# Optimization experiments

Measured on AMD Instinct MI355X. Metric: run time of the kernel, lower is better.

The kernel has to match this reference:

```python
import jax, jax.numpy as jnp
import numpy as np

# CUBA-LIF constants (from LavaNetwork.__init__ with beta=0.95)
THRESHOLD = 1.0
CURRENT_DECAY = 1.0   # current[t] = (1-1.0)*current[t-1] + input[t] == input[t]
VOLTAGE_DECAY = 1.0 - 0.95  # = 0.05, so v[t] = 0.95*v[t-1] + cur[t]

N_INPUT, N_HIDDEN, N_OUTPUT = 512, 2048, 4 * 64
B, T = 32, 1024


def setup_inputs() -> dict:
    key = jax.random.key(0)
    kx, k1, k2, k3, k4 = jax.random.split(key, 5)
    x = (jax.random.uniform(kx, (B, N_INPUT, T)) < 0.1).astype(jnp.float32)
    # learned params (Linear with bias); small scale so spiking is reasonable
    w1 = jax.random.normal(k1, (N_HIDDEN, N_INPUT), dtype=jnp.float32) * (1.0 / np.sqrt(N_INPUT))
    b1 = jax.random.normal(k2, (N_HIDDEN,), dtype=jnp.float32) * 0.01
    w2 = jax.random.normal(k3, (N_OUTPUT, N_HIDDEN), dtype=jnp.float32) * (1.0 / np.sqrt(N_HIDDEN))
    b2 = jax.random.normal(k4, (N_OUTPUT,), dtype=jnp.float32) * 0.01
    return {"x": x, "w1": w1, "b1": b1, "w2": w2, "b2": b2}


def _cuba_lif(cur):
    """CUBA neuron with current_decay=1 (current==synaptic input),
    leaky-integrate voltage, fire at threshold, reset voltage to 0.
    cur: (B, N, T) -> spikes (B, N, T)."""
    beta_v = 1.0 - VOLTAGE_DECAY  # 0.95

    def step(v, c_t):
        v = v * beta_v + c_t
        s = (v >= THRESHOLD).astype(v.dtype)
        v = v * (1.0 - s)  # reset-to-zero on spike (Loihi behavior)
        return v, s

    cur_t = jnp.moveaxis(cur, -1, 0)  # (T, B, N)
    v0 = jnp.zeros(cur.shape[:-1], cur.dtype)
    _, spk = jax.lax.scan(step, v0, cur_t)
    return jnp.moveaxis(spk, 0, -1)  # (B, N, T)


def reference(x, w1, b1, w2, b2):
    # layer 1: synapse (einsum 'bit,oi->bot' + bias) -> CUBA neuron
    cur1 = jnp.einsum('bit,oi->bot', x, w1) + b1[None, :, None]
    spk1 = _cuba_lif(cur1)
    # layer 2
    cur2 = jnp.einsum('bit,oi->bot', spk1, w2) + b2[None, :, None]
    spk2 = _cuba_lif(cur2)
    return (spk1, spk2)
```

## Files before the change

### kernel.cpp

```cpp
#include <hip/hip_runtime.h>


typedef int i32x4 __attribute__((ext_vector_type(4)));
typedef _Float16 f16x8 __attribute__((ext_vector_type(8)));
typedef _Float16 f16x4 __attribute__((ext_vector_type(4)));
typedef float f32x4 __attribute__((ext_vector_type(4)));

#define GLDS(g, l) __builtin_amdgcn_global_load_lds( \
    (const __attribute__((address_space(1))) void*)(g), \
    (__attribute__((address_space(3))) void*)(l), 16, 0, 0)

#define INV231 4.656612873077392578125e-10


__global__ __launch_bounds__(256) void prep_w8(const float* __restrict__ A,
                                               signed char* __restrict__ wp,
                                               int M, int K)
{
    long gt = (long)blockIdx.x * 256 + threadIdx.x;
    int kq4 = K >> 2;
    int m = (int)(gt / kq4), kq = (int)(gt % kq4);
    int k0 = kq * 4;
    int kt = k0 >> 6, kin = k0 & 63;
    int cw = ((kin >> 4) ^ (m >> 1)) & 3;
    float4 w = *(const float4*)&A[(long)m * K + k0];
    float wv[4] = {w.x, w.y, w.z, w.w};
    int pack[4] = {0, 0, 0, 0};
#pragma unroll
    for (int e = 0; e < 4; e++) {
        long k64 = (long)rint((double)wv[e] * 2147483648.0);
#pragma unroll
        for (int j = 0; j < 3; j++) {
            long r = ((k64 + 128) & 255) - 128;
            pack[j] |= ((int)r & 255) << (e * 8);
            k64 = (k64 - r) >> 8;
        }
        pack[3] |= ((int)k64 & 255) << (e * 8);
    }
#pragma unroll
    for (int p = 0; p < 4; p++)
        *(int*)&wp[(((long)kt * 4 + p) * M + m) * 64 + cw * 16 + (kin & 15)] = pack[p];
}

__global__ __launch_bounds__(256) void prep_x8(const float* __restrict__ x,
                                               unsigned char* __restrict__ xt)
{
    __shared__ float xs[64][68];
    const int b = blockIdx.z, i0 = blockIdx.y * 64, t0 = blockIdx.x * 64;
    const float* xb = x + ((long)b * 512 + i0) * 1024 + t0;
#pragma unroll
    for (int p = 0; p < 4; p++) {
        int f = threadIdx.x + p * 256;
        int i = f >> 4, t4 = (f & 15) * 4;
        *(float4*)&xs[i][t4] = *(const float4*)&xb[(long)i * 1024 + t4];
    }
    __syncthreads();
    int tt = threadIdx.x >> 2, c = threadIdx.x & 3;
    unsigned char bytes[16];
#pragma unroll
    for (int j = 0; j < 16; j++)
        bytes[j] = (unsigned char)xs[c * 16 + j][tt];
    *(uint4*)&xt[(((long)b * 8 + (i0 >> 6)) * 1024 + t0 + tt) * 64 + c * 16] =
        *(uint4*)bytes;
}

template <bool TRANS>
__global__ __launch_bounds__(256, 3) void gemm_i8(
    const signed char* __restrict__ wp,
    const unsigned char* __restrict__ act,
    const float* __restrict__ bias,
    float* __restrict__ C,
    int M, int K)
{
    __shared__ signed char Ws[2][4][32][64];

    const int b = blockIdx.z;
    const int m0 = blockIdx.x * 32, t0 = blockIdx.y * 128;
    const int tid = threadIdx.x, lane = tid & 63, wave = tid >> 6;
    const int wt = t0 + wave * 32;
    const int lm = lane & 15, lq = lane >> 4;
    const int fro = ((lq ^ (lm >> 1)) & 3) * 16;
    const int gl_t = lane >> 2, gl_c = (lane & 3) * 16;
    const int niter = K >> 6;

    const unsigned char* ab = act + (long)b * niter * 1024 * 64;
    const int p0 = wave >> 1, s0 = wave & 1;
    const int p1 = (wave + 4) >> 1, s1 = wave & 1;

    i32x4 acc[4][2][2];
#pragma unroll
    for (int p = 0; p < 4; p++)
#pragma unroll
        for (int i = 0; i < 2; i++)
#pragma unroll
            for (int j = 0; j < 2; j++) acc[p][i][j] = (i32x4)0;

    {
        const signed char* g0 = wp + (((long)p0) * M + m0 + s0 * 16 + gl_t) * 64 + gl_c;
        const signed char* g1 = wp + (((long)p1) * M + m0 + s1 * 16 + gl_t) * 64 + gl_c;
        GLDS(g0, &Ws[0][p0][s0 * 16][0]);
        GLDS(g1, &Ws[0][p1][s1 * 16][0]);
    }
    i32x4 a0 = *(const i32x4*)&ab[((long)(wt + 0 * 16 + lm)) * 64 + lq * 16];
    i32x4 a1 = *(const i32x4*)&ab[((long)(wt + 1 * 16 + lm)) * 64 + lq * 16];
    __syncthreads();

    for (int it = 0; it < niter; it++) {
        const int buf = it & 1;
        const int nx = (it + 1 < niter) ? it + 1 : it;
        if (it + 1 < niter) {
            const long kb = (long)(it + 1) * 4;
            const signed char* g0 =
                wp + ((kb + p0) * M + m0 + s0 * 16 + gl_t) * 64 + gl_c;
            const signed char* g1 =
                wp + ((kb + p1) * M + m0 + s1 * 16 + gl_t) * 64 + gl_c;
            GLDS(g0, &Ws[buf ^ 1][p0][s0 * 16][0]);
            GLDS(g1, &Ws[buf ^ 1][p1][s1 * 16][0]);
        }
        i32x4 an0 = *(const i32x4*)&ab[((long)nx * 1024 + wt + 0 * 16 + lm) * 64 + lq * 16];
        i32x4 an1 = *(const i32x4*)&ab[((long)nx * 1024 + wt + 1 * 16 + lm) * 64 + lq * 16];

#pragma unroll
        for (int p = 0; p < 4; p++) {
            i32x4 w0 = *(const i32x4*)&Ws[buf][p][lm][fro];
            i32x4 w1 = *(const i32x4*)&Ws[buf][p][16 + lm][fro];
            if (TRANS) {
                acc[p][0][0] = __builtin_amdgcn_mfma_i32_16x16x64_i8(a0, w0, acc[p][0][0], 0, 0, 0);
                acc[p][0][1] = __builtin_amdgcn_mfma_i32_16x16x64_i8(a0, w1, acc[p][0][1], 0, 0, 0);
                acc[p][1][0] = __builtin_amdgcn_mfma_i32_16x16x64_i8(a1, w0, acc[p][1][0], 0, 0, 0);
                acc[p][1][1] = __builtin_amdgcn_mfma_i32_16x16x64_i8(a1, w1, acc[p][1][1], 0, 0, 0);
            } else {
                acc[p][0][0] = __builtin_amdgcn_mfma_i32_16x16x64_i8(w0, a0, acc[p][0][0], 0, 0, 0);
                acc[p][0][1] = __builtin_amdgcn_mfma_i32_16x16x64_i8(w0, a1, acc[p][0][1], 0, 0, 0);
                acc[p][1][0] = __builtin_amdgcn_mfma_i32_16x16x64_i8(w1, a0, acc[p][1][0], 0, 0, 0);
                acc[p][1][1] = __builtin_amdgcn_mfma_i32_16x16x64_i8(w1, a1, acc[p][1][1], 0, 0, 0);
            }
        }
        __syncthreads();
        a0 = an0; a1 = an1;
    }

    if (TRANS) {
        double bv[2];
        bv[0] = (double)bias[m0 + lm];
        bv[1] = (double)bias[m0 + 16 + lm];
        float* Cb = C + (long)b * 1024 * M;
#pragma unroll
        for (int tf = 0; tf < 2; tf++)
#pragma unroll
            for (int r = 0; r < 4; r++) {
                const int trow = wt + tf * 16 + lq * 4 + r;
#pragma unroll
                for (int mf = 0; mf < 2; mf++) {
                    long T = acc[3][tf][mf][r];
                    T = T * 256 + acc[2][tf][mf][r];
                    T = T * 256 + acc[1][tf][mf][r];
                    T = T * 256 + acc[0][tf][mf][r];
                    Cb[(long)trow * M + m0 + mf * 16 + lm] =
                        (float)((double)T * INV231 + bv[mf]);
                }
            }
    } else {
        float* Cb = C + (long)b * M * 1024;
#pragma unroll
        for (int mf = 0; mf < 2; mf++)
#pragma unroll
            for (int r = 0; r < 4; r++) {
                const int mrow = m0 + mf * 16 + lq * 4 + r;
                const double bv = (double)bias[mrow];
#pragma unroll
                for (int tf = 0; tf < 2; tf++) {
                    long T = acc[3][mf][tf][r];
                    T = T * 256 + acc[2][mf][tf][r];
                    T = T * 256 + acc[1][mf][tf][r];
                    T = T * 256 + acc[0][mf][tf][r];
                    Cb[(long)mrow * 1024 + wt + tf * 16 + lm] =
                        (float)((double)T * INV231 + bv);
                }
            }
    }
}


__global__ __launch_bounds__(256) void lif1_t(
    const float* __restrict__ ct,
    unsigned char* __restrict__ spk8,
    unsigned* __restrict__ mask_ws)
{
    const int b = blockIdx.y;
    const int m = blockIdx.x * 256 + threadIdx.x;
    const float* src = ct + (long)b * 1024 * 2048 + m;
    unsigned char* spb = spk8 + (((long)b * 32 + (m >> 6)) * 1024) * 64 + (m & 63);
    unsigned* mw = mask_ws + (long)b * 32 * 2048 + m;
    double v = 0.0;
    for (int tw = 0; tw < 32; tw++) {
        float c[32];
#pragma unroll
        for (int j = 0; j < 32; j++)
            c[j] = src[(long)(tw * 32 + j) * 2048];
        unsigned mword = 0;
#pragma unroll
        for (int j = 0; j < 32; j++) {
            v = 0.95 * v + (double)c[j];
            bool s = v >= 1.0;
            mword |= (s ? 1u : 0u) << j;
            if (s) v = 0.0;
            spb[(long)(tw * 32 + j) * 64] = s ? 1 : 0;
        }
        mw[(long)tw * 2048] = mword;
    }
}

__global__ __launch_bounds__(256) void expand_spk(
    const unsigned* __restrict__ mask_ws,
    float* __restrict__ spk1)
{
    __shared__ unsigned msk[8][32];
    const long rowbase = (long)blockIdx.x * 8;
    const int b = (int)(rowbase >> 11), m0 = (int)(rowbase & 2047);
    const int tid = threadIdx.x;
    {
        int w = tid >> 3, r = tid & 7;
        msk[r][w] = mask_ws[((long)b * 32 + w) * 2048 + m0 + r];
    }
    __syncthreads();
    const int r = tid >> 5, l5 = tid & 31;
    float* dst = spk1 + (rowbase + r) * 1024;
    const int sh = (l5 & 7) * 4;
#pragma unroll
    for (int j = 0; j < 8; j++) {
        const int t = l5 * 4 + j * 128;
        const unsigned w = msk[r][(l5 >> 3) + j * 4];
        float4 o;
        o.x = ((w >> sh) & 1u) ? 1.f : 0.f;
        o.y = ((w >> (sh + 1)) & 1u) ? 1.f : 0.f;
        o.z = ((w >> (sh + 2)) & 1u) ? 1.f : 0.f;
        o.w = ((w >> (sh + 3)) & 1u) ? 1.f : 0.f;
        *(float4*)&dst[t] = o;
    }
}

template <int RPB>
__global__ __launch_bounds__(256) void lif_lds(float* __restrict__ cur)
{
    __shared__ float cs[RPB][36];
    const long rowbase = (long)blockIdx.x * RPB;
    float* base = cur + rowbase * 1024;
    const int tid = threadIdx.x;
    double v = 0.0;
    const int NV = RPB * 32 / 4;
    for (int tc = 0; tc < 1024; tc += 32) {
        for (int f = tid; f < NV; f += 256) {
            int row = f >> 3, t4 = (f & 7) * 4;
            *(float4*)&cs[row][t4] = *(const float4*)&base[(long)row * 1024 + tc + t4];
        }
        __syncthreads();
        if (tid < RPB) {
#pragma unroll
            for (int j = 0; j < 32; j++) {
                v = 0.95 * v + (double)cs[tid][j];
                bool s = v >= 1.0;
                cs[tid][j] = s ? 1.f : 0.f;
                if (s) v = 0.0;
            }
        }
        __syncthreads();
        for (int f = tid; f < NV; f += 256) {
            int row = f >> 3, t4 = (f & 7) * 4;
            *(float4*)&base[(long)row * 1024 + tc + t4] = *(float4*)&cs[row][t4];
        }
        __syncthreads();
    }
}


__device__ inline void split3(float w, _Float16& q0, _Float16& q1, _Float16& q2) {
    float p0 = rintf(w * 4096.f) * 2.44140625e-4f;
    float r1 = w - p0;
    float p1s = rintf(r1 * 8388608.f) * 2.44140625e-4f;
    float r2 = r1 - p1s * 4.8828125e-4f;
    float p2s = rintf(r2 * 1.7179869184e10f) * 1.220703125e-4f;
    q0 = (_Float16)p0; q1 = (_Float16)p1s; q2 = (_Float16)p2s;
}

__global__ __launch_bounds__(256) void gemm_f16x3_kernel(
    const float* __restrict__ A, const float* __restrict__ Bmat,
    const float* __restrict__ bias, float* __restrict__ C,
    int M, int N, int K, long sB, long sC)
{
    __shared__ _Float16 As[3][128][40];
    __shared__ _Float16 Bsh[128][40];
    const int batch = blockIdx.z;
    const float* Bp = Bmat + (long)batch * sB;
    float* Cp = C + (long)batch * sC;
    const int m0 = blockIdx.y * 128, n0 = blockIdx.x * 128;
    const int tid = threadIdx.x, lane = tid & 63, wave = tid >> 6;
    const int wrow = (wave >> 1) * 64, wcol = (wave & 1) * 64;
    const int lm = lane & 15, lq = lane >> 4;
    const int a_mo = tid >> 3, a_kc = (tid & 7) * 4;
    const int b_kq = tid >> 5, b_nq = tid & 31;

    f32x4 acc[3][4][4];
#pragma unroll
    for (int p = 0; p < 3; p++)
#pragma unroll
        for (int i = 0; i < 4; i++)
#pragma unroll
            for (int j = 0; j < 4; j++) acc[p][i][j] = (f32x4)0.f;

    for (int k0 = 0; k0 < K; k0 += 32) {
#pragma unroll
        for (int i = 0; i < 4; i++) {
            const int m = i * 32 + a_mo;
            float4 w = *(const float4*)&A[(long)(m0 + m) * K + k0 + a_kc];
            _Float16 a0[4], a1[4], a2[4];
            split3(w.x, a0[0], a1[0], a2[0]);
            split3(w.y, a0[1], a1[1], a2[1]);
            split3(w.z, a0[2], a1[2], a2[2]);
            split3(w.w, a0[3], a1[3], a2[3]);
            *(f16x4*)&As[0][m][a_kc] = (f16x4){a0[0], a0[1], a0[2], a0[3]};
            *(f16x4*)&As[1][m][a_kc] = (f16x4){a1[0], a1[1], a1[2], a1[3]};
            *(f16x4*)&As[2][m][a_kc] = (f16x4){a2[0], a2[1], a2[2], a2[3]};
        }
        {
            float4 r0 = *(const float4*)&Bp[(long)(k0 + b_kq * 4 + 0) * N + n0 + b_nq * 4];
            float4 r1 = *(const float4*)&Bp[(long)(k0 + b_kq * 4 + 1) * N + n0 + b_nq * 4];
            float4 r2 = *(const float4*)&Bp[(long)(k0 + b_kq * 4 + 2) * N + n0 + b_nq * 4];
            float4 r3 = *(const float4*)&Bp[(long)(k0 + b_kq * 4 + 3) * N + n0 + b_nq * 4];
            *(f16x4*)&Bsh[b_nq * 4 + 0][b_kq * 4] =
                (f16x4){(_Float16)r0.x, (_Float16)r1.x, (_Float16)r2.x, (_Float16)r3.x};
            *(f16x4*)&Bsh[b_nq * 4 + 1][b_kq * 4] =
                (f16x4){(_Float16)r0.y, (_Float16)r1.y, (_Float16)r2.y, (_Float16)r3.y};
            *(f16x4*)&Bsh[b_nq * 4 + 2][b_kq * 4] =
                (f16x4){(_Float16)r0.z, (_Float16)r1.z, (_Float16)r2.z, (_Float16)r3.z};
            *(f16x4*)&Bsh[b_nq * 4 + 3][b_kq * 4] =
                (f16x4){(_Float16)r0.w, (_Float16)r1.w, (_Float16)r2.w, (_Float16)r3.w};
        }
        __syncthreads();
        f16x8 bf[4];
#pragma unroll
        for (int j = 0; j < 4; j++)
            bf[j] = *(const f16x8*)&Bsh[wcol + j * 16 + lm][lq * 8];
#pragma unroll
        for (int p = 0; p < 3; p++) {
            f16x8 af[4];
#pragma unroll
            for (int i = 0; i < 4; i++)
                af[i] = *(const f16x8*)&As[p][wrow + i * 16 + lm][lq * 8];
#pragma unroll
            for (int i = 0; i < 4; i++)
#pragma unroll
                for (int j = 0; j < 4; j++)
                    acc[p][i][j] = __builtin_amdgcn_mfma_f32_16x16x32_f16(
                        af[i], bf[j], acc[p][i][j], 0, 0, 0);
        }
        __syncthreads();
    }
#pragma unroll
    for (int i = 0; i < 4; i++)
#pragma unroll
        for (int r = 0; r < 4; r++) {
            const int row = m0 + wrow + i * 16 + lq * 4 + r;
            const double bv = (double)bias[row];
#pragma unroll
            for (int j = 0; j < 4; j++) {
                double s = (double)acc[0][i][j][r]
                         + (double)acc[1][i][j][r] * 4.8828125e-4
                         + (double)acc[2][i][j][r] * 4.76837158203125e-7 + bv;
                Cp[(long)row * N + n0 + wcol + j * 16 + lm] = (float)s;
            }
        }
}

__global__ __launch_bounds__(256) void lif_rows(float* __restrict__ data,
                                                long nrows, int T)
{
    long r = (long)blockIdx.x * blockDim.x + threadIdx.x;
    if (r >= nrows) return;
    float* p = data + r * (long)T;
    double v = 0.0;
    for (int t = 0; t < T; t += 4) {
        float4 c = *(float4*)(p + t);
        float4 s;
        v = 0.95 * v + (double)c.x; s.x = (v >= 1.0) ? 1.f : 0.f; if (v >= 1.0) v = 0.0;
        v = 0.95 * v + (double)c.y; s.y = (v >= 1.0) ? 1.f : 0.f; if (v >= 1.0) v = 0.0;
        v = 0.95 * v + (double)c.z; s.z = (v >= 1.0) ? 1.f : 0.f; if (v >= 1.0) v = 0.0;
        v = 0.95 * v + (double)c.w; s.w = (v >= 1.0) ? 1.f : 0.f; if (v >= 1.0) v = 0.0;
        *(float4*)(p + t) = s;
    }
}


extern "C" void kernel_launch(void* const* d_in, const int* in_sizes, int n_in,
                              void* d_out, int out_size, void* d_ws, size_t ws_size,
                              hipStream_t stream)
{
    const float* x  = (const float*)d_in[0];
    const float* w1 = (const float*)d_in[1];
    const float* b1 = (const float*)d_in[2];
    const float* w2 = (const float*)d_in[3];
    const float* b2 = (const float*)d_in[4];

    float* out  = (float*)d_out;
    float* spk1 = out;
    float* spk2 = out + (long)32 * 2048 * 1024;

    const size_t WP1 = 4194304;
    const size_t WP2 = 2097152;
    const size_t X8T = 16777216;
    const size_t SPK = 67108864;
    const size_t MSK = 8388608;
    const size_t NEED = WP1 + WP2 + X8T + SPK + MSK;

    if (ws_size >= NEED) {
        char* ws = (char*)d_ws;
        signed char* wp1 = (signed char*)ws;
        signed char* wp2 = (signed char*)(ws + WP1);
        unsigned char* x8t = (unsigned char*)(ws + WP1 + WP2);
        unsigned char* spk8 = (unsigned char*)(ws + WP1 + WP2 + X8T);
        unsigned* mask_ws = (unsigned*)(ws + WP1 + WP2 + X8T + SPK);

        prep_w8<<<1024, 256, 0, stream>>>(w1, wp1, 2048, 512);
        prep_w8<<<512, 256, 0, stream>>>(w2, wp2, 256, 2048);
        prep_x8<<<dim3(16, 8, 32), 256, 0, stream>>>(x, x8t);

        gemm_i8<true><<<dim3(64, 8, 32), 256, 0, stream>>>(
            wp1, x8t, b1, spk1, 2048, 512);
        lif1_t<<<dim3(8, 32), 256, 0, stream>>>(spk1, spk8, mask_ws);
        expand_spk<<<8192, 256, 0, stream>>>(mask_ws, spk1);

        gemm_i8<false><<<dim3(8, 8, 32), 256, 0, stream>>>(
            wp2, spk8, b2, spk2, 256, 2048);
        lif_lds<128><<<64, 256, 0, stream>>>(spk2);
    } else {
        gemm_f16x3_kernel<<<dim3(8, 16, 32), 256, 0, stream>>>(
            w1, x, b1, spk1, 2048, 1024, 512, (long)512 * 1024, (long)2048 * 1024);
        lif_rows<<<(65536 + 255) / 256, 256, 0, stream>>>(spk1, 65536, 1024);
        gemm_f16x3_kernel<<<dim3(8, 2, 32), 256, 0, stream>>>(
            w2, spk1, b2, spk2, 256, 1024, 2048, (long)2048 * 1024, (long)256 * 1024);
        lif_rows<<<(8192 + 255) / 256, 256, 0, stream>>>(spk2, 8192, 1024);
    }
}
```

Before: 735.8 us.

## Widen int8 GEMM time tile, prefetch LIF inputs, and retune LIF2 grid

The int8 MFMA GEMM now has each wave cover 64 time steps instead of 32, so each block tile spans 256 time steps. Every LDS weight fragment feeds twice as many MFMAs, and the grid is reordered so blocks that share the same time slice and batch run close together. lif1_t double-buffers its column loads so the next 32 time steps are fetched while the current ones are integrated, and the layer-2 LIF launches 256 blocks of 32 rows instead of 64 blocks of 128. The cost is a larger accumulator and register footprint, with launch bounds lowered from 3 to 2 blocks per CU to make room, which reduces occupancy.

```diff
diff --git a/kernel.cpp b/kernel.cpp
--- a/kernel.cpp
+++ b/kernel.cpp
@@ -65,7 +65,7 @@
 }
 
 template <bool TRANS>
-__global__ __launch_bounds__(256, 3) void gemm_i8(
+__global__ __launch_bounds__(256, 2) void gemm_i8(
     const signed char* __restrict__ wp,
     const unsigned char* __restrict__ act,
     const float* __restrict__ bias,
@@ -74,10 +74,10 @@
 {
     __shared__ signed char Ws[2][4][32][64];
 
-    const int b = blockIdx.z;
-    const int m0 = blockIdx.x * 32, t0 = blockIdx.y * 128;
+    const int b = blockIdx.y;
+    const int m0 = blockIdx.z * 32, t0 = blockIdx.x * 256;
     const int tid = threadIdx.x, lane = tid & 63, wave = tid >> 6;
-    const int wt = t0 + wave * 32;
+    const int wt = t0 + wave * 64;
     const int lm = lane & 15, lq = lane >> 4;
     const int fro = ((lq ^ (lm >> 1)) & 3) * 16;
     const int gl_t = lane >> 2, gl_c = (lane & 3) * 16;
@@ -87,13 +87,11 @@
     const int p0 = wave >> 1, s0 = wave & 1;
     const int p1 = (wave + 4) >> 1, s1 = wave & 1;
 
-    i32x4 acc[4][2][2];
+    i32x4 acc[4][8];
 #pragma unroll
     for (int p = 0; p < 4; p++)
 #pragma unroll
-        for (int i = 0; i < 2; i++)
-#pragma unroll
-            for (int j = 0; j < 2; j++) acc[p][i][j] = (i32x4)0;
+        for (int q = 0; q < 8; q++) acc[p][q] = (i32x4)0;
 
     {
         const signed char* g0 = wp + (((long)p0) * M + m0 + s0 * 16 + gl_t) * 64 + gl_c;
@@ -101,8 +99,10 @@
         GLDS(g0, &Ws[0][p0][s0 * 16][0]);
         GLDS(g1, &Ws[0][p1][s1 * 16][0]);
     }
-    i32x4 a0 = *(const i32x4*)&ab[((long)(wt + 0 * 16 + lm)) * 64 + lq * 16];
-    i32x4 a1 = *(const i32x4*)&ab[((long)(wt + 1 * 16 + lm)) * 64 + lq * 16];
+    i32x4 a[4], an[4];
+#pragma unroll
+    for (int f = 0; f < 4; f++)
+        a[f] = *(const i32x4*)&ab[((long)(wt + f * 16 + lm)) * 64 + lq * 16];
     __syncthreads();
 
     for (int it = 0; it < niter; it++) {
@@ -117,27 +117,35 @@
             GLDS(g0, &Ws[buf ^ 1][p0][s0 * 16][0]);
             GLDS(g1, &Ws[buf ^ 1][p1][s1 * 16][0]);
         }
-        i32x4 an0 = *(const i32x4*)&ab[((long)nx * 1024 + wt + 0 * 16 + lm) * 64 + lq * 16];
-        i32x4 an1 = *(const i32x4*)&ab[((long)nx * 1024 + wt + 1 * 16 + lm) * 64 + lq * 16];
+#pragma unroll
+        for (int f = 0; f < 4; f++)
+            an[f] = *(const i32x4*)&ab[((long)nx * 1024 + wt + f * 16 + lm) * 64 + lq * 16];
 
 #pragma unroll
         for (int p = 0; p < 4; p++) {
             i32x4 w0 = *(const i32x4*)&Ws[buf][p][lm][fro];
             i32x4 w1 = *(const i32x4*)&Ws[buf][p][16 + lm][fro];
             if (TRANS) {
-                acc[p][0][0] = __builtin_amdgcn_mfma_i32_16x16x64_i8(a0, w0, acc[p][0][0], 0, 0, 0);
-                acc[p][0][1] = __builtin_amdgcn_mfma_i32_16x16x64_i8(a0, w1, acc[p][0][1], 0, 0, 0);
-                acc[p][1][0] = __builtin_amdgcn_mfma_i32_16x16x64_i8(a1, w0, acc[p][1][0], 0, 0, 0);
-                acc[p][1][1] = __builtin_amdgcn_mfma_i32_16x16x64_i8(a1, w1, acc[p][1][1], 0, 0, 0);
+#pragma unroll
+                for (int f = 0; f < 4; f++) {
+                    acc[p][f * 2 + 0] = __builtin_amdgcn_mfma_i32_16x16x64_i8(
+                        a[f], w0, acc[p][f * 2 + 0], 0, 0, 0);
+                    acc[p][f * 2 + 1] = __builtin_amdgcn_mfma_i32_16x16x64_i8(
+                        a[f], w1, acc[p][f * 2 + 1], 0, 0, 0);
+                }
             } else {
-                acc[p][0][0] = __builtin_amdgcn_mfma_i32_16x16x64_i8(w0, a0, acc[p][0][0], 0, 0, 0);
-                acc[p][0][1] = __builtin_amdgcn_mfma_i32_16x16x64_i8(w0, a1, acc[p][0][1], 0, 0, 0);
-                acc[p][1][0] = __builtin_amdgcn_mfma_i32_16x16x64_i8(w1, a0, acc[p][1][0], 0, 0, 0);
-                acc[p][1][1] = __builtin_amdgcn_mfma_i32_16x16x64_i8(w1, a1, acc[p][1][1], 0, 0, 0);
+#pragma unroll
+                for (int f = 0; f < 4; f++) {
+                    acc[p][0 + f] = __builtin_amdgcn_mfma_i32_16x16x64_i8(
+                        w0, a[f], acc[p][0 + f], 0, 0, 0);
+                    acc[p][4 + f] = __builtin_amdgcn_mfma_i32_16x16x64_i8(
+                        w1, a[f], acc[p][4 + f], 0, 0, 0);
+                }
             }
         }
         __syncthreads();
-        a0 = an0; a1 = an1;
+#pragma unroll
+        for (int f = 0; f < 4; f++) a[f] = an[f];
     }
 
     if (TRANS) {
@@ -146,16 +154,16 @@
         bv[1] = (double)bias[m0 + 16 + lm];
         float* Cb = C + (long)b * 1024 * M;
 #pragma unroll
-        for (int tf = 0; tf < 2; tf++)
+        for (int tf = 0; tf < 4; tf++)
 #pragma unroll
             for (int r = 0; r < 4; r++) {
                 const int trow = wt + tf * 16 + lq * 4 + r;
 #pragma unroll
                 for (int mf = 0; mf < 2; mf++) {
-                    long T = acc[3][tf][mf][r];
-                    T = T * 256 + acc[2][tf][mf][r];
-                    T = T * 256 + acc[1][tf][mf][r];
-                    T = T * 256 + acc[0][tf][mf][r];
+                    long T = acc[3][tf * 2 + mf][r];
+                    T = T * 256 + acc[2][tf * 2 + mf][r];
+                    T = T * 256 + acc[1][tf * 2 + mf][r];
+                    T = T * 256 + acc[0][tf * 2 + mf][r];
                     Cb[(long)trow * M + m0 + mf * 16 + lm] =
                         (float)((double)T * INV231 + bv[mf]);
                 }
@@ -169,11 +177,11 @@
                 const int mrow = m0 + mf * 16 + lq * 4 + r;
                 const double bv = (double)bias[mrow];
 #pragma unroll
-                for (int tf = 0; tf < 2; tf++) {
-                    long T = acc[3][mf][tf][r];
-                    T = T * 256 + acc[2][mf][tf][r];
-                    T = T * 256 + acc[1][mf][tf][r];
-                    T = T * 256 + acc[0][mf][tf][r];
+                for (int tf = 0; tf < 4; tf++) {
+                    long T = acc[3][mf * 4 + tf][r];
+                    T = T * 256 + acc[2][mf * 4 + tf][r];
+                    T = T * 256 + acc[1][mf * 4 + tf][r];
+                    T = T * 256 + acc[0][mf * 4 + tf][r];
                     Cb[(long)mrow * 1024 + wt + tf * 16 + lm] =
                         (float)((double)T * INV231 + bv);
                 }
@@ -193,21 +201,39 @@
     unsigned char* spb = spk8 + (((long)b * 32 + (m >> 6)) * 1024) * 64 + (m & 63);
     unsigned* mw = mask_ws + (long)b * 32 * 2048 + m;
     double v = 0.0;
-    for (int tw = 0; tw < 32; tw++) {
-        float c[32];
+    float c0[32], c1[32];
+#pragma unroll
+    for (int j = 0; j < 32; j++)
+        c0[j] = src[(long)j * 2048];
+    for (int tw = 0; tw < 32; tw += 2) {
 #pragma unroll
         for (int j = 0; j < 32; j++)
-            c[j] = src[(long)(tw * 32 + j) * 2048];
+            c1[j] = src[(long)((tw + 1) * 32 + j) * 2048];
         unsigned mword = 0;
 #pragma unroll
         for (int j = 0; j < 32; j++) {
-            v = 0.95 * v + (double)c[j];
+            v = 0.95 * v + (double)c0[j];
             bool s = v >= 1.0;
             mword |= (s ? 1u : 0u) << j;
             if (s) v = 0.0;
             spb[(long)(tw * 32 + j) * 64] = s ? 1 : 0;
         }
         mw[(long)tw * 2048] = mword;
+        if (tw + 2 < 32) {
+#pragma unroll
+            for (int j = 0; j < 32; j++)
+                c0[j] = src[(long)((tw + 2) * 32 + j) * 2048];
+        }
+        mword = 0;
+#pragma unroll
+        for (int j = 0; j < 32; j++) {
+            v = 0.95 * v + (double)c1[j];
+            bool s = v >= 1.0;
+            mword |= (s ? 1u : 0u) << j;
+            if (s) v = 0.0;
+            spb[(long)((tw + 1) * 32 + j) * 64] = s ? 1 : 0;
+        }
+        mw[(long)(tw + 1) * 2048] = mword;
     }
 }
 
@@ -424,14 +450,14 @@
         prep_w8<<<512, 256, 0, stream>>>(w2, wp2, 256, 2048);
         prep_x8<<<dim3(16, 8, 32), 256, 0, stream>>>(x, x8t);
 
-        gemm_i8<true><<<dim3(64, 8, 32), 256, 0, stream>>>(
+        gemm_i8<true><<<dim3(4, 32, 64), 256, 0, stream>>>(
             wp1, x8t, b1, spk1, 2048, 512);
         lif1_t<<<dim3(8, 32), 256, 0, stream>>>(spk1, spk8, mask_ws);
         expand_spk<<<8192, 256, 0, stream>>>(mask_ws, spk1);
 
-        gemm_i8<false><<<dim3(8, 8, 32), 256, 0, stream>>>(
+        gemm_i8<false><<<dim3(4, 32, 8), 256, 0, stream>>>(
             wp2, spk8, b2, spk2, 256, 2048);
-        lif_lds<128><<<64, 256, 0, stream>>>(spk2);
+        lif_lds<32><<<256, 256, 0, stream>>>(spk2);
     } else {
         gemm_f16x3_kernel<<<dim3(8, 16, 32), 256, 0, stream>>>(
             w1, x, b1, spk1, 2048, 1024, 512, (long)512 * 1024, (long)2048 * 1024);
```

Measured after the change: 743.4 us. About the same (+1.0%).
